# Kernel tuning notes

Hardware: AMD Instinct MI355X
Metric: run time of the kernel (lower is better)

Reference implementation:

```python
import jax, jax.numpy as jnp
import numpy as np
import math

N_HEAD = 32
ROPE_BASE = 10000.0


def _rope_headwise(x):
    # Faithful to the source bug: x is [B, H, S, D] and the rotary module uses
    # x.shape[1] (= H) as the "sequence length", so the angle depends on the
    # head index, broadcast over the true sequence axis.
    B, H, S, D = x.shape
    inv_freq = 1.0 / (ROPE_BASE ** (jnp.arange(0, D, 2, dtype=jnp.float32) / D))  # [D/2]
    t = jnp.arange(H, dtype=jnp.float32)                                          # [H]
    freqs = t[:, None] * inv_freq[None, :]                                        # [H, D/2]
    # emb = cat(freqs, freqs)[..., :D//2] == freqs, so cos/sin are just over freqs
    cos = jnp.cos(freqs)[None, :, None, :]   # [1, H, 1, D/2]
    sin = jnp.sin(freqs)[None, :, None, :]
    x1, x2 = x[..., : D // 2], x[..., D // 2 :]
    return jnp.concatenate([x1 * cos - x2 * sin, x1 * sin + x2 * cos], axis=-1)


def setup_inputs() -> dict:
    key = jax.random.key(0)
    ks = jax.random.split(key, 5)
    B, S, E = 2, 2048, 2048
    scale = 0.02
    return {
        "x": jax.random.normal(ks[0], (B, S, E), dtype=jnp.float32),
        "Wq": jax.random.normal(ks[1], (E, E), dtype=jnp.float32) * scale,
        "bq": jnp.zeros((E,), dtype=jnp.float32),
        "Wk": jax.random.normal(ks[2], (E, E), dtype=jnp.float32) * scale,
        "bk": jnp.zeros((E,), dtype=jnp.float32),
        "Wv": jax.random.normal(ks[3], (E, E), dtype=jnp.float32) * scale,
        "bv": jnp.zeros((E,), dtype=jnp.float32),
        "Wo": jax.random.normal(ks[4], (E, E), dtype=jnp.float32) * scale,
        "bo": jnp.zeros((E,), dtype=jnp.float32),
    }


def reference(x, Wq, bq, Wk, bk, Wv, bv, Wo, bo):
    B, S, E = x.shape
    H = N_HEAD
    D = E // H

    def split_heads(y):  # [B,S,E] -> [B,H,S,D]
        return y.reshape(B, S, H, D).transpose(0, 2, 1, 3)

    q = split_heads(x @ Wq + bq)
    k = split_heads(x @ Wk + bk)
    v = split_heads(x @ Wv + bv)

    q = _rope_headwise(q)
    k = _rope_headwise(k)

    scores = jnp.einsum("bhqd,bhkd->bhqk", q, k) / math.sqrt(D)  # [B,H,S,S]
    causal = jnp.triu(jnp.ones((S, S), dtype=bool), k=1)
    scores = jnp.where(causal[None, None], -jnp.inf, scores)
    attn = jax.nn.softmax(scores, axis=-1)
    out = jnp.einsum("bhqk,bhkd->bhqd", attn, v)                 # [B,H,S,D]
    out = out.transpose(0, 2, 1, 3).reshape(B, S, E)
    return out @ Wo + bo
```

## Files before the change

### kernel.cpp

```cpp
#include <hip/hip_runtime.h>
#include <hip/hip_bf16.h>

#define B_ 2
#define S_ 2048
#define E_ 2048
#define H_ 32
#define M_ (B_*S_)

typedef __bf16 bf16x8 __attribute__((ext_vector_type(8)));
typedef float  f32x4  __attribute__((ext_vector_type(4)));

__device__ __forceinline__ ushort f2bf(float f) {
    uint u = __float_as_uint(f);
    u += 0x7fffu + ((u >> 16) & 1u);
    return (ushort)(u >> 16);
}
__device__ __forceinline__ float bf2f(ushort h) {
    return __uint_as_float(((uint)h) << 16);
}
__device__ __forceinline__ f32x4 f4zero() {
    f32x4 z; z[0]=0.f; z[1]=0.f; z[2]=0.f; z[3]=0.f; return z;
}
__device__ __forceinline__ void async16(const ushort* g, ushort* l) {
    __builtin_amdgcn_global_load_lds((const __attribute__((address_space(1))) void*)g,
                                     (__attribute__((address_space(3))) void*)l, 16, 0, 0);
}

__global__ __launch_bounds__(256) void cast_x_kernel(const float* __restrict__ x,
                                                     ushort* __restrict__ xb) {
    int i = (blockIdx.x * 256 + threadIdx.x) * 4;
    float4 v = *(const float4*)(x + i);
    ushort4 o;
    o.x = f2bf(v.x); o.y = f2bf(v.y); o.z = f2bf(v.z); o.w = f2bf(v.w);
    *(ushort4*)(xb + i) = o;
}

__global__ __launch_bounds__(256) void wtrans_kernel(const float* __restrict__ W0, const float* __restrict__ W1,
                                                     const float* __restrict__ W2, const float* __restrict__ W3,
                                                     ushort* __restrict__ T0, ushort* __restrict__ T1,
                                                     ushort* __restrict__ T2, ushort* __restrict__ T3) {
    const float* W = (blockIdx.z==0)?W0:(blockIdx.z==1)?W1:(blockIdx.z==2)?W2:W3;
    ushort*      T = (blockIdx.z==0)?T0:(blockIdx.z==1)?T1:(blockIdx.z==2)?T2:T3;
    __shared__ float tile[64][65];
    int k0 = blockIdx.y * 64, n0 = blockIdx.x * 64;
    int tx = threadIdx.x & 63, ty = threadIdx.x >> 6;
    #pragma unroll
    for (int it = 0; it < 16; ++it) {
        int r = it * 4 + ty;
        tile[r][tx] = W[(size_t)(k0 + r) * E_ + n0 + tx];
    }
    __syncthreads();
    #pragma unroll
    for (int it = 0; it < 16; ++it) {
        int r = it * 4 + ty;
        T[(size_t)(n0 + r) * E_ + k0 + tx] = f2bf(tile[tx][r]);
    }
}

__global__ __launch_bounds__(256) void vtrans_kernel(const ushort* __restrict__ vb,
                                                     ushort* __restrict__ vt) {
    __shared__ ushort tile[64][65];
    const int bh = blockIdx.y, b = bh >> 5, h = bh & 31;
    const int s0 = blockIdx.x * 64;
    int tx = threadIdx.x & 63, ty = threadIdx.x >> 6;
    #pragma unroll
    for (int it = 0; it < 16; ++it) {
        int r = it * 4 + ty;
        tile[r][tx] = vb[(size_t)(b * S_ + s0 + r) * E_ + h * 64 + tx];
    }
    __syncthreads();
    #pragma unroll
    for (int it = 0; it < 16; ++it) {
        int r = it * 4 + ty;
        vt[(size_t)(bh * 64 + r) * S_ + s0 + tx] = tile[tx][r];
    }
}

template<bool OUTF32, bool DOROPE>
__global__ __launch_bounds__(256) void gemm128(const ushort* __restrict__ A,
        const ushort* __restrict__ Bt0, const ushort* __restrict__ Bt1, const ushort* __restrict__ Bt2,
        const float* __restrict__ bias0, const float* __restrict__ bias1, const float* __restrict__ bias2,
        void* __restrict__ C0, void* __restrict__ C1, void* __restrict__ C2) {
    const ushort* Bt  = (blockIdx.z==0)?Bt0:(blockIdx.z==1)?Bt1:Bt2;
    const float* bias = (blockIdx.z==0)?bias0:(blockIdx.z==1)?bias1:bias2;
    void* Cv          = (blockIdx.z==0)?C0:(blockIdx.z==1)?C1:C2;

    __shared__ ushort As[128 * 64];
    __shared__ ushort Bs[128 * 64];

    const int tid  = threadIdx.x;
    const int wave = tid >> 6, lane = tid & 63;
    const int quad = lane >> 4, l15 = lane & 15;
    const int wm = wave >> 1, wn = wave & 1;
    const int m0 = blockIdx.y * 128, n0 = blockIdx.x * 128;
    const int srow = tid >> 3;
    const int scgx = (tid & 7) ^ (srow & 7);

    f32x4 acc[4][4];
    #pragma unroll
    for (int i = 0; i < 4; ++i)
        #pragma unroll
        for (int j = 0; j < 4; ++j) acc[i][j] = f4zero();

    for (int k0 = 0; k0 < E_; k0 += 64) {
        #pragma unroll
        for (int it = 0; it < 4; ++it) {
            int r = it * 32 + srow;
            async16(A  + (size_t)(m0 + r) * E_ + k0 + scgx * 8, As + (it * 256 + wave * 64) * 8);
            async16(Bt + (size_t)(n0 + r) * E_ + k0 + scgx * 8, Bs + (it * 256 + wave * 64) * 8);
        }
        __syncthreads();
        #pragma unroll
        for (int kk = 0; kk < 2; ++kk) {
            bf16x8 af[4], bfr[4];
            #pragma unroll
            for (int mt = 0; mt < 4; ++mt) {
                int row = wm * 64 + mt * 16 + l15;
                af[mt] = *(const bf16x8*)(As + row * 64 + (((kk * 4 + quad) ^ (row & 7)) << 3));
            }
            #pragma unroll
            for (int nt = 0; nt < 4; ++nt) {
                int row = wn * 64 + nt * 16 + l15;
                bfr[nt] = *(const bf16x8*)(Bs + row * 64 + (((kk * 4 + quad) ^ (row & 7)) << 3));
            }
            #pragma unroll
            for (int mt = 0; mt < 4; ++mt)
                #pragma unroll
                for (int nt = 0; nt < 4; ++nt)
                    acc[mt][nt] = __builtin_amdgcn_mfma_f32_16x16x32_bf16(af[mt], bfr[nt], acc[mt][nt], 0, 0, 0);
        }
        __syncthreads();
    }

    if (DOROPE && blockIdx.z != 2) {
        const float qsc = (blockIdx.z == 0) ? 0.125f : 1.0f;
        const int h = (n0 + wn * 64) >> 6;
        float sn[2], cs[2];
        #pragma unroll
        for (int nt = 0; nt < 2; ++nt) {
            int j = nt * 16 + l15;
            float ang = (float)h * __expf(-(float)j * 0.28782313662425575f);
            __sincosf(ang, &sn[nt], &cs[nt]);
        }
        ushort* C = (ushort*)Cv;
        #pragma unroll
        for (int mt = 0; mt < 4; ++mt) {
            #pragma unroll
            for (int nt = 0; nt < 2; ++nt) {
                int col1 = n0 + wn * 64 + nt * 16 + l15;
                float b1 = bias[col1], b2 = bias[col1 + 32];
                #pragma unroll
                for (int r = 0; r < 4; ++r) {
                    int rowg = m0 + wm * 64 + mt * 16 + quad * 4 + r;
                    float x1 = acc[mt][nt][r] + b1;
                    float x2 = acc[mt][nt + 2][r] + b2;
                    C[(size_t)rowg * E_ + col1]      = f2bf((x1 * cs[nt] - x2 * sn[nt]) * qsc);
                    C[(size_t)rowg * E_ + col1 + 32] = f2bf((x1 * sn[nt] + x2 * cs[nt]) * qsc);
                }
            }
        }
    } else {
        #pragma unroll
        for (int mt = 0; mt < 4; ++mt) {
            #pragma unroll
            for (int nt = 0; nt < 4; ++nt) {
                int col = n0 + wn * 64 + nt * 16 + l15;
                float bv = bias[col];
                #pragma unroll
                for (int r = 0; r < 4; ++r) {
                    int rowg = m0 + wm * 64 + mt * 16 + quad * 4 + r;
                    float v = acc[mt][nt][r] + bv;
                    if (OUTF32) ((float*)Cv)[(size_t)rowg * E_ + col] = v;
                    else        ((ushort*)Cv)[(size_t)rowg * E_ + col] = f2bf(v);
                }
            }
        }
    }
}

__global__ __launch_bounds__(256) void flash_kernel(const ushort* __restrict__ qb,
        const ushort* __restrict__ kb, const ushort* __restrict__ vt,
        ushort* __restrict__ ctx) {
    __shared__ ushort KVs[2][2][64 * 64];
    __shared__ ushort Ps[4][32 * 64];

    const int tid  = threadIdx.x;
    const int wave = tid >> 6, lane = tid & 63;
    const int quad = lane >> 4, l15 = lane & 15;
    const int bh = blockIdx.y, b = bh >> 5, h = bh & 31;
    const int srow = tid >> 3;
    const int scgx = (tid & 7) ^ (srow & 7);
    ushort* Pw = Ps[wave];

    bf16x8 ones;
    #pragma unroll
    for (int j = 0; j < 8; ++j) ones[j] = (__bf16)1.0f;

    #pragma unroll 1
    for (int pass = 0; pass < 2; ++pass) {
        const int qx  = pass ? (15 - (int)blockIdx.x) : (int)blockIdx.x;
        const int q0  = qx * 128;
        const int qw0 = q0 + wave * 32;
        const int nkt = 2 * qx + 2;

        bf16x8 qf[2][2];
        #pragma unroll
        for (int mt = 0; mt < 2; ++mt)
            #pragma unroll
            for (int kk = 0; kk < 2; ++kk)
                qf[mt][kk] = *(const bf16x8*)(qb + (size_t)(b * S_ + qw0 + mt * 16 + l15) * E_ + h * 64 + kk * 32 + quad * 8);

        f32x4 oacc[2][4], lacc[2];
        #pragma unroll
        for (int mt = 0; mt < 2; ++mt) {
            lacc[mt] = f4zero();
            #pragma unroll
            for (int dt = 0; dt < 4; ++dt) oacc[mt][dt] = f4zero();
        }

        #pragma unroll
        for (int it = 0; it < 2; ++it) {
            int r = it * 32 + srow;
            async16(kb + (size_t)(b * S_ + r) * E_ + h * 64 + scgx * 8, KVs[0][0] + (it * 256 + wave * 64) * 8);
            async16(vt + (size_t)(bh * 64 + r) * S_ + scgx * 8,         KVs[0][1] + (it * 256 + wave * 64) * 8);
        }
        __syncthreads();

        #pragma unroll 1
        for (int kt = 0; kt < nkt; ++kt) {
            const int k0 = kt * 64;
            if (kt + 1 < nkt) {
                const int kn = k0 + 64;
                ushort* Kd = KVs[(kt + 1) & 1][0];
                ushort* Vd = KVs[(kt + 1) & 1][1];
                #pragma unroll
                for (int it = 0; it < 2; ++it) {
                    int r = it * 32 + srow;
                    async16(kb + (size_t)(b * S_ + kn + r) * E_ + h * 64 + scgx * 8, Kd + (it * 256 + wave * 64) * 8);
                    async16(vt + (size_t)(bh * 64 + r) * S_ + kn + scgx * 8,         Vd + (it * 256 + wave * 64) * 8);
                }
            }

            if (k0 <= qw0 + 31) {
                const ushort* Ks = KVs[kt & 1][0];
                const ushort* Vs = KVs[kt & 1][1];
                f32x4 sacc[2][4];
                #pragma unroll
                for (int mt = 0; mt < 2; ++mt)
                    #pragma unroll
                    for (int nt = 0; nt < 4; ++nt) sacc[mt][nt] = f4zero();
                #pragma unroll
                for (int kk = 0; kk < 2; ++kk)
                    #pragma unroll
                    for (int nt = 0; nt < 4; ++nt) {
                        int row = nt * 16 + l15;
                        bf16x8 kf = *(const bf16x8*)(Ks + row * 64 + (((kk * 4 + quad) ^ (row & 7)) << 3));
                        #pragma unroll
                        for (int mt = 0; mt < 2; ++mt)
                            sacc[mt][nt] = __builtin_amdgcn_mfma_f32_16x16x32_bf16(kf, qf[mt][kk], sacc[mt][nt], 0, 0, 0);
                    }

                #pragma unroll
                for (int mt = 0; mt < 2; ++mt) {
                    const int q  = qw0 + mt * 16 + l15;
                    const bool dm = (k0 + 63 > qw0 + mt * 16);
                    const int ql = mt * 16 + l15, swz = ql & 7;
                    #pragma unroll
                    for (int nt = 0; nt < 4; ++nt) {
                        ushort4 pk;
                        #pragma unroll
                        for (int r = 0; r < 4; ++r) {
                            int s = k0 + nt * 16 + quad * 4 + r;
                            float p = __expf(sacc[mt][nt][r]);
                            if (dm && s > q) p = 0.f;
                            ((ushort*)&pk)[r] = f2bf(p);
                        }
                        *(ushort4*)(Pw + ql * 64 + (((nt * 2 + (quad >> 1)) ^ swz) << 3) + (quad & 1) * 4) = pk;
                    }
                }

                #pragma unroll
                for (int kk = 0; kk < 2; ++kk) {
                    bf16x8 pf[2];
                    #pragma unroll
                    for (int mt = 0; mt < 2; ++mt) {
                        int ql = mt * 16 + l15;
                        pf[mt] = *(const bf16x8*)(Pw + ql * 64 + (((kk * 4 + quad) ^ (ql & 7)) << 3));
                    }
                    #pragma unroll
                    for (int mt = 0; mt < 2; ++mt)
                        lacc[mt] = __builtin_amdgcn_mfma_f32_16x16x32_bf16(pf[mt], ones, lacc[mt], 0, 0, 0);
                    #pragma unroll
                    for (int dt = 0; dt < 4; ++dt) {
                        int row = dt * 16 + l15;
                        bf16x8 vf = *(const bf16x8*)(Vs + row * 64 + (((kk * 4 + quad) ^ (row & 7)) << 3));
                        #pragma unroll
                        for (int mt = 0; mt < 2; ++mt)
                            oacc[mt][dt] = __builtin_amdgcn_mfma_f32_16x16x32_bf16(pf[mt], vf, oacc[mt][dt], 0, 0, 0);
                    }
                }
            }
            __syncthreads();
        }

        #pragma unroll
        for (int mt = 0; mt < 2; ++mt)
            #pragma unroll
            for (int r = 0; r < 4; ++r) {
                float inv = 1.0f / lacc[mt][r];
                #pragma unroll
                for (int dt = 0; dt < 4; ++dt)
                    ctx[(size_t)(b * S_ + qw0 + mt * 16 + quad * 4 + r) * E_ + h * 64 + dt * 16 + l15] =
                        f2bf(oacc[mt][dt][r] * inv);
            }
    }
}

extern "C" void kernel_launch(void* const* d_in, const int* in_sizes, int n_in,
                              void* d_out, int out_size, void* d_ws, size_t ws_size,
                              hipStream_t stream) {
    const float* x  = (const float*)d_in[0];
    const float* Wq = (const float*)d_in[1];
    const float* bq = (const float*)d_in[2];
    const float* Wk = (const float*)d_in[3];
    const float* bk = (const float*)d_in[4];
    const float* Wv = (const float*)d_in[5];
    const float* bv = (const float*)d_in[6];
    const float* Wo = (const float*)d_in[7];
    const float* bo = (const float*)d_in[8];
    float* out = (float*)d_out;

    ushort* p   = (ushort*)d_ws;
    ushort* xb  = p; p += (size_t)M_ * E_;
    ushort* wqt = p; p += (size_t)E_ * E_;
    ushort* wkt = p; p += (size_t)E_ * E_;
    ushort* wvt = p; p += (size_t)E_ * E_;
    ushort* wot = p; p += (size_t)E_ * E_;
    ushort* qb  = p; p += (size_t)M_ * E_;
    ushort* kb  = p; p += (size_t)M_ * E_;
    ushort* vb  = p; p += (size_t)M_ * E_;
    ushort* ctx = p; p += (size_t)M_ * E_;
    ushort* vt  = xb;

    cast_x_kernel<<<(M_ * E_) / 1024, 256, 0, stream>>>(x, xb);
    wtrans_kernel<<<dim3(E_ / 64, E_ / 64, 4), 256, 0, stream>>>(Wq, Wk, Wv, Wo, wqt, wkt, wvt, wot);
    gemm128<false, true><<<dim3(E_ / 128, M_ / 128, 3), 256, 0, stream>>>(
        xb, wqt, wkt, wvt, bq, bk, bv, qb, kb, vb);
    vtrans_kernel<<<dim3(S_ / 64, B_ * H_), 256, 0, stream>>>(vb, vt);
    flash_kernel<<<dim3(8, B_ * H_), 256, 0, stream>>>(qb, kb, vt, ctx);
    gemm128<true, false><<<dim3(E_ / 128, M_ / 128, 1), 256, 0, stream>>>(
        ctx, wot, wot, wot, bo, bo, bo, out, out, out);
}
```

Measured before the change: 409.0 us.

## Split flash blocks per query tile, linearize GEMM grid, vectorize bf16 packing

The flash kernel now launches one block per query tile, with heaviest tiles first, instead of pairing two tiles per block in a balanced two-pass loop. That doubles the block count and drops per-block serialization, at the cost of uneven per-block work. The GEMM grid is flattened so Q/K/V blocks sharing the same A rows and N tile are interleaved for better L2 reuse. The weight transpose and cast kernels use float4 loads and packed bf16x2 conversions, and the P-tile packing uses the packed conversion too.

```diff
diff --git a/kernel.cpp b/kernel.cpp
--- a/kernel.cpp
+++ b/kernel.cpp
@@ -15,6 +15,10 @@
     u += 0x7fffu + ((u >> 16) & 1u);
     return (ushort)(u >> 16);
 }
+__device__ __forceinline__ uint pack2bf(float a, float b) {
+    __hip_bfloat162 h = __float22bfloat162_rn(make_float2(a, b));
+    return *(uint*)&h;
+}
 __device__ __forceinline__ float bf2f(ushort h) {
     return __uint_as_float(((uint)h) << 16);
 }
@@ -30,9 +34,10 @@
                                                      ushort* __restrict__ xb) {
     int i = (blockIdx.x * 256 + threadIdx.x) * 4;
     float4 v = *(const float4*)(x + i);
-    ushort4 o;
-    o.x = f2bf(v.x); o.y = f2bf(v.y); o.z = f2bf(v.z); o.w = f2bf(v.w);
-    *(ushort4*)(xb + i) = o;
+    uint2 o;
+    o.x = pack2bf(v.x, v.y);
+    o.y = pack2bf(v.z, v.w);
+    *(uint2*)(xb + i) = o;
 }
 
 __global__ __launch_bounds__(256) void wtrans_kernel(const float* __restrict__ W0, const float* __restrict__ W1,
@@ -42,18 +47,23 @@
     const float* W = (blockIdx.z==0)?W0:(blockIdx.z==1)?W1:(blockIdx.z==2)?W2:W3;
     ushort*      T = (blockIdx.z==0)?T0:(blockIdx.z==1)?T1:(blockIdx.z==2)?T2:T3;
     __shared__ float tile[64][65];
-    int k0 = blockIdx.y * 64, n0 = blockIdx.x * 64;
-    int tx = threadIdx.x & 63, ty = threadIdx.x >> 6;
-    #pragma unroll
-    for (int it = 0; it < 16; ++it) {
-        int r = it * 4 + ty;
-        tile[r][tx] = W[(size_t)(k0 + r) * E_ + n0 + tx];
+    const int k0 = blockIdx.y * 64, n0 = blockIdx.x * 64;
+    const int rr = threadIdx.x >> 4;
+    const int cc = (threadIdx.x & 15) * 4;
+    #pragma unroll
+    for (int p = 0; p < 4; ++p) {
+        int r = p * 16 + rr;
+        float4 v = *(const float4*)(W + (size_t)(k0 + r) * E_ + n0 + cc);
+        tile[r][cc+0] = v.x; tile[r][cc+1] = v.y; tile[r][cc+2] = v.z; tile[r][cc+3] = v.w;
     }
     __syncthreads();
     #pragma unroll
-    for (int it = 0; it < 16; ++it) {
-        int r = it * 4 + ty;
-        T[(size_t)(n0 + r) * E_ + k0 + tx] = f2bf(tile[tx][r]);
+    for (int p = 0; p < 4; ++p) {
+        int rn = p * 16 + rr;
+        uint2 o;
+        o.x = pack2bf(tile[cc+0][rn], tile[cc+1][rn]);
+        o.y = pack2bf(tile[cc+2][rn], tile[cc+3][rn]);
+        *(uint2*)(T + (size_t)(n0 + rn) * E_ + k0 + cc) = o;
     }
 }
 
@@ -76,14 +86,19 @@
     }
 }
 
-template<bool OUTF32, bool DOROPE>
+template<bool OUTF32, bool DOROPE, int NZ>
 __global__ __launch_bounds__(256) void gemm128(const ushort* __restrict__ A,
         const ushort* __restrict__ Bt0, const ushort* __restrict__ Bt1, const ushort* __restrict__ Bt2,
         const float* __restrict__ bias0, const float* __restrict__ bias1, const float* __restrict__ bias2,
         void* __restrict__ C0, void* __restrict__ C1, void* __restrict__ C2) {
-    const ushort* Bt  = (blockIdx.z==0)?Bt0:(blockIdx.z==1)?Bt1:Bt2;
-    const float* bias = (blockIdx.z==0)?bias0:(blockIdx.z==1)?bias1:bias2;
-    void* Cv          = (blockIdx.z==0)?C0:(blockIdx.z==1)?C1:C2;
+    const int bid = blockIdx.x;
+    const int z   = bid % NZ;
+    const int nb  = (bid / NZ) % (E_ / 128);
+    const int mb  = bid / (NZ * (E_ / 128));
+
+    const ushort* Bt  = (z==0)?Bt0:(z==1)?Bt1:Bt2;
+    const float* bias = (z==0)?bias0:(z==1)?bias1:bias2;
+    void* Cv          = (z==0)?C0:(z==1)?C1:C2;
 
     __shared__ ushort As[128 * 64];
     __shared__ ushort Bs[128 * 64];
@@ -92,7 +107,7 @@
     const int wave = tid >> 6, lane = tid & 63;
     const int quad = lane >> 4, l15 = lane & 15;
     const int wm = wave >> 1, wn = wave & 1;
-    const int m0 = blockIdx.y * 128, n0 = blockIdx.x * 128;
+    const int m0 = mb * 128, n0 = nb * 128;
     const int srow = tid >> 3;
     const int scgx = (tid & 7) ^ (srow & 7);
 
@@ -132,8 +147,8 @@
         __syncthreads();
     }
 
-    if (DOROPE && blockIdx.z != 2) {
-        const float qsc = (blockIdx.z == 0) ? 0.125f : 1.0f;
+    if (DOROPE && z != 2) {
+        const float qsc = (z == 0) ? 0.125f : 1.0f;
         const int h = (n0 + wn * 64) >> 6;
         float sn[2], cs[2];
         #pragma unroll
@@ -196,124 +211,123 @@
     #pragma unroll
     for (int j = 0; j < 8; ++j) ones[j] = (__bf16)1.0f;
 
+    const int qx  = 15 - (int)blockIdx.x;
+    const int q0  = qx * 128;
+    const int qw0 = q0 + wave * 32;
+    const int nkt = 2 * qx + 2;
+
+    bf16x8 qf[2][2];
+    #pragma unroll
+    for (int mt = 0; mt < 2; ++mt)
+        #pragma unroll
+        for (int kk = 0; kk < 2; ++kk)
+            qf[mt][kk] = *(const bf16x8*)(qb + (size_t)(b * S_ + qw0 + mt * 16 + l15) * E_ + h * 64 + kk * 32 + quad * 8);
+
+    f32x4 oacc[2][4], lacc[2];
+    #pragma unroll
+    for (int mt = 0; mt < 2; ++mt) {
+        lacc[mt] = f4zero();
+        #pragma unroll
+        for (int dt = 0; dt < 4; ++dt) oacc[mt][dt] = f4zero();
+    }
+
+    #pragma unroll
+    for (int it = 0; it < 2; ++it) {
+        int r = it * 32 + srow;
+        async16(kb + (size_t)(b * S_ + r) * E_ + h * 64 + scgx * 8, KVs[0][0] + (it * 256 + wave * 64) * 8);
+        async16(vt + (size_t)(bh * 64 + r) * S_ + scgx * 8,         KVs[0][1] + (it * 256 + wave * 64) * 8);
+    }
+    __syncthreads();
+
     #pragma unroll 1
-    for (int pass = 0; pass < 2; ++pass) {
-        const int qx  = pass ? (15 - (int)blockIdx.x) : (int)blockIdx.x;
-        const int q0  = qx * 128;
-        const int qw0 = q0 + wave * 32;
-        const int nkt = 2 * qx + 2;
-
-        bf16x8 qf[2][2];
-        #pragma unroll
-        for (int mt = 0; mt < 2; ++mt)
+    for (int kt = 0; kt < nkt; ++kt) {
+        const int k0 = kt * 64;
+        if (kt + 1 < nkt) {
+            const int kn = k0 + 64;
+            ushort* Kd = KVs[(kt + 1) & 1][0];
+            ushort* Vd = KVs[(kt + 1) & 1][1];
+            #pragma unroll
+            for (int it = 0; it < 2; ++it) {
+                int r = it * 32 + srow;
+                async16(kb + (size_t)(b * S_ + kn + r) * E_ + h * 64 + scgx * 8, Kd + (it * 256 + wave * 64) * 8);
+                async16(vt + (size_t)(bh * 64 + r) * S_ + kn + scgx * 8,         Vd + (it * 256 + wave * 64) * 8);
+            }
+        }
+
+        if (k0 <= qw0 + 31) {
+            const ushort* Ks = KVs[kt & 1][0];
+            const ushort* Vs = KVs[kt & 1][1];
+            f32x4 sacc[2][4];
+            #pragma unroll
+            for (int mt = 0; mt < 2; ++mt)
+                #pragma unroll
+                for (int nt = 0; nt < 4; ++nt) sacc[mt][nt] = f4zero();
             #pragma unroll
             for (int kk = 0; kk < 2; ++kk)
-                qf[mt][kk] = *(const bf16x8*)(qb + (size_t)(b * S_ + qw0 + mt * 16 + l15) * E_ + h * 64 + kk * 32 + quad * 8);
-
-        f32x4 oacc[2][4], lacc[2];
-        #pragma unroll
-        for (int mt = 0; mt < 2; ++mt) {
-            lacc[mt] = f4zero();
-            #pragma unroll
-            for (int dt = 0; dt < 4; ++dt) oacc[mt][dt] = f4zero();
-        }
-
-        #pragma unroll
-        for (int it = 0; it < 2; ++it) {
-            int r = it * 32 + srow;
-            async16(kb + (size_t)(b * S_ + r) * E_ + h * 64 + scgx * 8, KVs[0][0] + (it * 256 + wave * 64) * 8);
-            async16(vt + (size_t)(bh * 64 + r) * S_ + scgx * 8,         KVs[0][1] + (it * 256 + wave * 64) * 8);
-        }
-        __syncthreads();
-
-        #pragma unroll 1
-        for (int kt = 0; kt < nkt; ++kt) {
-            const int k0 = kt * 64;
-            if (kt + 1 < nkt) {
-                const int kn = k0 + 64;
-                ushort* Kd = KVs[(kt + 1) & 1][0];
-                ushort* Vd = KVs[(kt + 1) & 1][1];
-                #pragma unroll
-                for (int it = 0; it < 2; ++it) {
-                    int r = it * 32 + srow;
-                    async16(kb + (size_t)(b * S_ + kn + r) * E_ + h * 64 + scgx * 8, Kd + (it * 256 + wave * 64) * 8);
-                    async16(vt + (size_t)(bh * 64 + r) * S_ + kn + scgx * 8,         Vd + (it * 256 + wave * 64) * 8);
-                }
-            }
-
-            if (k0 <= qw0 + 31) {
-                const ushort* Ks = KVs[kt & 1][0];
-                const ushort* Vs = KVs[kt & 1][1];
-                f32x4 sacc[2][4];
-                #pragma unroll
-                for (int mt = 0; mt < 2; ++mt)
-                    #pragma unroll
-                    for (int nt = 0; nt < 4; ++nt) sacc[mt][nt] = f4zero();
-                #pragma unroll
-                for (int kk = 0; kk < 2; ++kk)
-                    #pragma unroll
-                    for (int nt = 0; nt < 4; ++nt) {
-                        int row = nt * 16 + l15;
-                        bf16x8 kf = *(const bf16x8*)(Ks + row * 64 + (((kk * 4 + quad) ^ (row & 7)) << 3));
-                        #pragma unroll
-                        for (int mt = 0; mt < 2; ++mt)
-                            sacc[mt][nt] = __builtin_amdgcn_mfma_f32_16x16x32_bf16(kf, qf[mt][kk], sacc[mt][nt], 0, 0, 0);
-                    }
-
-                #pragma unroll
-                for (int mt = 0; mt < 2; ++mt) {
-                    const int q  = qw0 + mt * 16 + l15;
-                    const bool dm = (k0 + 63 > qw0 + mt * 16);
-                    const int ql = mt * 16 + l15, swz = ql & 7;
-                    #pragma unroll
-                    for (int nt = 0; nt < 4; ++nt) {
-                        ushort4 pk;
-                        #pragma unroll
-                        for (int r = 0; r < 4; ++r) {
-                            int s = k0 + nt * 16 + quad * 4 + r;
-                            float p = __expf(sacc[mt][nt][r]);
-                            if (dm && s > q) p = 0.f;
-                            ((ushort*)&pk)[r] = f2bf(p);
-                        }
-                        *(ushort4*)(Pw + ql * 64 + (((nt * 2 + (quad >> 1)) ^ swz) << 3) + (quad & 1) * 4) = pk;
-                    }
-                }
-
-                #pragma unroll
-                for (int kk = 0; kk < 2; ++kk) {
-                    bf16x8 pf[2];
-                    #pragma unroll
-                    for (int mt = 0; mt < 2; ++mt) {
-                        int ql = mt * 16 + l15;
-                        pf[mt] = *(const bf16x8*)(Pw + ql * 64 + (((kk * 4 + quad) ^ (ql & 7)) << 3));
-                    }
+                #pragma unroll
+                for (int nt = 0; nt < 4; ++nt) {
+                    int row = nt * 16 + l15;
+                    bf16x8 kf = *(const bf16x8*)(Ks + row * 64 + (((kk * 4 + quad) ^ (row & 7)) << 3));
                     #pragma unroll
                     for (int mt = 0; mt < 2; ++mt)
-                        lacc[mt] = __builtin_amdgcn_mfma_f32_16x16x32_bf16(pf[mt], ones, lacc[mt], 0, 0, 0);
+                        sacc[mt][nt] = __builtin_amdgcn_mfma_f32_16x16x32_bf16(kf, qf[mt][kk], sacc[mt][nt], 0, 0, 0);
+                }
+
+            #pragma unroll
+            for (int mt = 0; mt < 2; ++mt) {
+                const int q  = qw0 + mt * 16 + l15;
+                const bool dm = (k0 + 63 > qw0 + mt * 16);
+                const int ql = mt * 16 + l15, swz = ql & 7;
+                #pragma unroll
+                for (int nt = 0; nt < 4; ++nt) {
+                    float p[4];
                     #pragma unroll
-                    for (int dt = 0; dt < 4; ++dt) {
-                        int row = dt * 16 + l15;
-                        bf16x8 vf = *(const bf16x8*)(Vs + row * 64 + (((kk * 4 + quad) ^ (row & 7)) << 3));
-                        #pragma unroll
-                        for (int mt = 0; mt < 2; ++mt)
-                            oacc[mt][dt] = __builtin_amdgcn_mfma_f32_16x16x32_bf16(pf[mt], vf, oacc[mt][dt], 0, 0, 0);
+                    for (int r = 0; r < 4; ++r) {
+                        int s = k0 + nt * 16 + quad * 4 + r;
+                        p[r] = __expf(sacc[mt][nt][r]);
+                        if (dm && s > q) p[r] = 0.f;
                     }
-                }
-            }
-            __syncthreads();
-        }
-
-        #pragma unroll
-        for (int mt = 0; mt < 2; ++mt)
-            #pragma unroll
-            for (int r = 0; r < 4; ++r) {
-                float inv = 1.0f / lacc[mt][r];
-                #pragma unroll
-                for (int dt = 0; dt < 4; ++dt)
-                    ctx[(size_t)(b * S_ + qw0 + mt * 16 + quad * 4 + r) * E_ + h * 64 + dt * 16 + l15] =
-                        f2bf(oacc[mt][dt][r] * inv);
-            }
-    }
+                    uint2 pk;
+                    pk.x = pack2bf(p[0], p[1]);
+                    pk.y = pack2bf(p[2], p[3]);
+                    *(uint2*)(Pw + ql * 64 + (((nt * 2 + (quad >> 1)) ^ swz) << 3) + (quad & 1) * 4) = pk;
+                }
+            }
+
+            #pragma unroll
+            for (int kk = 0; kk < 2; ++kk) {
+                bf16x8 pf[2];
+                #pragma unroll
+                for (int mt = 0; mt < 2; ++mt) {
+                    int ql = mt * 16 + l15;
+                    pf[mt] = *(const bf16x8*)(Pw + ql * 64 + (((kk * 4 + quad) ^ (ql & 7)) << 3));
+                }
+                #pragma unroll
+                for (int mt = 0; mt < 2; ++mt)
+                    lacc[mt] = __builtin_amdgcn_mfma_f32_16x16x32_bf16(pf[mt], ones, lacc[mt], 0, 0, 0);
+                #pragma unroll
+                for (int dt = 0; dt < 4; ++dt) {
+                    int row = dt * 16 + l15;
+                    bf16x8 vf = *(const bf16x8*)(Vs + row * 64 + (((kk * 4 + quad) ^ (row & 7)) << 3));
+                    #pragma unroll
+                    for (int mt = 0; mt < 2; ++mt)
+                        oacc[mt][dt] = __builtin_amdgcn_mfma_f32_16x16x32_bf16(pf[mt], vf, oacc[mt][dt], 0, 0, 0);
+                }
+            }
+        }
+        __syncthreads();
+    }
+
+    #pragma unroll
+    for (int mt = 0; mt < 2; ++mt)
+        #pragma unroll
+        for (int r = 0; r < 4; ++r) {
+            float inv = 1.0f / lacc[mt][r];
+            #pragma unroll
+            for (int dt = 0; dt < 4; ++dt)
+                ctx[(size_t)(b * S_ + qw0 + mt * 16 + quad * 4 + r) * E_ + h * 64 + dt * 16 + l15] =
+                    f2bf(oacc[mt][dt][r] * inv);
+        }
 }
 
 extern "C" void kernel_launch(void* const* d_in, const int* in_sizes, int n_in,
@@ -344,10 +358,10 @@
 
     cast_x_kernel<<<(M_ * E_) / 1024, 256, 0, stream>>>(x, xb);
     wtrans_kernel<<<dim3(E_ / 64, E_ / 64, 4), 256, 0, stream>>>(Wq, Wk, Wv, Wo, wqt, wkt, wvt, wot);
-    gemm128<false, true><<<dim3(E_ / 128, M_ / 128, 3), 256, 0, stream>>>(
+    gemm128<false, true, 3><<<(E_ / 128) * (M_ / 128) * 3, 256, 0, stream>>>(
         xb, wqt, wkt, wvt, bq, bk, bv, qb, kb, vb);
     vtrans_kernel<<<dim3(S_ / 64, B_ * H_), 256, 0, stream>>>(vb, vt);
-    flash_kernel<<<dim3(8, B_ * H_), 256, 0, stream>>>(qb, kb, vt, ctx);
-    gemm128<true, false><<<dim3(E_ / 128, M_ / 128, 1), 256, 0, stream>>>(
+    flash_kernel<<<dim3(16, B_ * H_), 256, 0, stream>>>(qb, kb, vt, ctx);
+    gemm128<true, false, 1><<<(E_ / 128) * (M_ / 128), 256, 0, stream>>>(
         ctx, wot, wot, wot, bo, bo, bo, out, out, out);
 }
```

Result: slower. 437.2 us (+6.9%).
